# Performance work log

Hardware: AMD Instinct MI355X
Metric: run time of the kernel (lower is better)

Reference implementation:

```python
import jax, jax.numpy as jnp
import numpy as np

T, B, F, H, TAG = 512, 512, 128, 512, 2


def setup_inputs() -> dict:
    key = jax.random.key(0)
    ks = jax.random.split(key, 11)
    s = 1.0 / np.sqrt(H)  # PyTorch LSTMCell/Linear init scale
    u = lambda k, shape: jax.random.uniform(k, shape, jnp.float32, -s, s)
    return {
        "signal": jax.random.normal(ks[0], (T, B, F), jnp.float32),
        "W_ih1": u(ks[1], (4 * H, F)),
        "W_hh1": u(ks[2], (4 * H, H)),
        "b_ih1": u(ks[3], (4 * H,)),
        "b_hh1": u(ks[4], (4 * H,)),
        "W_ih2": u(ks[5], (4 * H, H)),
        "W_hh2": u(ks[6], (4 * H, H)),
        "b_ih2": u(ks[7], (4 * H,)),
        "b_hh2": u(ks[8], (4 * H,)),
        "W_lin": u(ks[9], (TAG, H)),
        "b_lin": u(ks[10], (TAG,)),
    }


def _lstm_cell(x, h, c, W_ih, W_hh, b_ih, b_hh):
    # PyTorch LSTMCell: gates = x W_ih^T + b_ih + h W_hh^T + b_hh; chunks i,f,g,o
    gates = x @ W_ih.T + h @ W_hh.T + (b_ih + b_hh)
    i, f, g, o = jnp.split(gates, 4, axis=-1)
    c_new = jax.nn.sigmoid(f) * c + jax.nn.sigmoid(i) * jnp.tanh(g)
    h_new = jax.nn.sigmoid(o) * jnp.tanh(c_new)
    return h_new, c_new


def reference(signal, W_ih1, W_hh1, b_ih1, b_hh1, W_ih2, W_hh2, b_ih2, b_hh2, W_lin, b_lin):
    n = signal.shape[1]
    hdim = W_hh1.shape[1]
    zeros = jnp.zeros((n, hdim), jnp.float32)

    def step(carry, x_t):
        h1, c1, h2, c2 = carry
        h1, c1 = _lstm_cell(x_t, h1, c1, W_ih1, W_hh1, b_ih1, b_hh1)
        h2, c2 = _lstm_cell(h1, h2, c2, W_ih2, W_hh2, b_ih2, b_hh2)
        out = h2 @ W_lin.T + b_lin  # [B, TAG]
        return (h1, c1, h2, c2), out

    _, outs = jax.lax.scan(step, (zeros, zeros, zeros, zeros), signal)
    # torch.cat(outputs, dim=1): list of T tensors [B, TAG] -> [B, T*TAG]
    t, b, tag = outs.shape
    return jnp.transpose(outs, (1, 0, 2)).reshape(b, t * tag)
```

## Files before the change

kernel.cpp:

```cpp
#include <hip/hip_runtime.h>
#include <hip/hip_fp16.h>
#include <stdint.h>

#define TSTEPS 512
#define BATCH  512
#define FEAT   128
#define HID    512
#define NGATE  2048

typedef _Float16 half8 __attribute__((ext_vector_type(8)));
typedef _Float16 half4v __attribute__((ext_vector_type(4)));
typedef float    floatx4 __attribute__((ext_vector_type(4)));

#define OFF_WIH1 0u
#define SZ_WIH1  ((unsigned)(NGATE*FEAT*2))
#define OFF_WHH1 (OFF_WIH1+SZ_WIH1)
#define SZ_WHH   ((unsigned)(NGATE*HID*2))
#define OFF_WIH2 (OFF_WHH1+SZ_WHH)
#define OFF_WHH2 (OFF_WIH2+SZ_WHH)
#define OFF_B1   (OFF_WHH2+SZ_WHH)
#define OFF_B2   (OFF_B1+(unsigned)(NGATE*4))
#define OFF_H1   (OFF_B2+(unsigned)(NGATE*4))
#define SZ_H     ((unsigned)(2*BATCH*HID*2))
#define OFF_H2   (OFF_H1+SZ_H)
#define OFF_C1   (OFF_H2+SZ_H)
#define SZ_C     ((unsigned)(BATCH*HID*4))
#define OFF_C2   (OFF_C1+SZ_C)
#define WS_END   (OFF_C2+SZ_C)

#define GLOBAL_AS __attribute__((address_space(1)))
#define LDS_AS    __attribute__((address_space(3)))

__device__ __forceinline__ void gload_lds16(const void* g, void* l) {
  __builtin_amdgcn_global_load_lds((const GLOBAL_AS void*)g, (LDS_AS void*)l, 16, 0, 0);
}

__device__ __forceinline__ half8 ldfrag(const _Float16* S, int r, int ko) {
  const int s = ko ^ (r & 3) ^ ((r >> 2) & 3);
  return *(const half8*)(S + r * 32 + s * 8);
}

__global__ void k_conv4(const float* __restrict__ s, _Float16* __restrict__ d, int n4) {
  int i = blockIdx.x * blockDim.x + threadIdx.x;
  if (i < n4) {
    const float4 v = ((const float4*)s)[i];
    half4v h; h[0] = (_Float16)v.x; h[1] = (_Float16)v.y; h[2] = (_Float16)v.z; h[3] = (_Float16)v.w;
    ((half4v*)d)[i] = h;
  }
}

__global__ void k_bias(const float* __restrict__ a, const float* __restrict__ b,
                       float* __restrict__ d, int n) {
  int i = blockIdx.x * blockDim.x + threadIdx.x;
  if (i < n) d[i] = a[i] + b[i];
}

template<bool XF32, int KX, bool DO_OUT>
__global__ __launch_bounds__(256)
void k_cell(const void* __restrict__ xsrc,
            const _Float16* __restrict__ Wx,
            const _Float16* __restrict__ Wh,
            const float* __restrict__ bias,
            const _Float16* __restrict__ hin,
            _Float16* __restrict__ hout,
            float* __restrict__ cst,
            const float* __restrict__ Wlin,
            const float* __restrict__ blin,
            float* __restrict__ out,
            int tstep)
{
  __shared__ __align__(16) _Float16 As[64 * 32];
  __shared__ __align__(16) _Float16 Bs[64 * 32];
  __shared__ float gs[64][65];
  __shared__ float hs[64][17];

  const int tid  = threadIdx.x;
  const int lane = tid & 63;
  const int wave = tid >> 6;
  const int wm = wave >> 1, wn = wave & 1;
  const int bx = blockIdx.x;
  const int hg = blockIdx.y;

  const int r_st  = tid >> 2;
  const int s_st  = tid & 3;
  const int ko_st = s_st ^ (r_st & 3) ^ ((r_st >> 2) & 3);
  const int arow  = bx * 64 + r_st;
  const int brow  = ((r_st >> 4) * HID) + hg * 16 + (r_st & 15);

  _Float16* AsW = As + wave * 512;
  _Float16* BsW = Bs + wave * 512;

  floatx4 acc[2][2];
  #pragma unroll
  for (int a = 0; a < 2; a++)
    #pragma unroll
    for (int b = 0; b < 2; b++) acc[a][b] = (floatx4){0.f, 0.f, 0.f, 0.f};

  const int fr_a = wm * 32 + (lane & 15);
  const int fr_b = wn * 32 + (lane & 15);
  const int fko  = lane >> 4;

  for (int kt = 0; kt < KX; kt += 32) {
    __syncthreads();
    if constexpr (XF32) {
      const float* xf = (const float*)xsrc + (size_t)arow * KX + kt + ko_st * 8;
      float4 v0 = *(const float4*)xf;
      float4 v1 = *(const float4*)(xf + 4);
      half8 h;
      h[0] = (_Float16)v0.x; h[1] = (_Float16)v0.y; h[2] = (_Float16)v0.z; h[3] = (_Float16)v0.w;
      h[4] = (_Float16)v1.x; h[5] = (_Float16)v1.y; h[6] = (_Float16)v1.z; h[7] = (_Float16)v1.w;
      *(half8*)(As + tid * 8) = h;
    } else {
      const _Float16* xh = (const _Float16*)xsrc + (size_t)arow * KX + kt + ko_st * 8;
      gload_lds16(xh, AsW);
    }
    gload_lds16(Wx + (size_t)brow * KX + kt + ko_st * 8, BsW);
    __syncthreads();
    half8 a0 = ldfrag(As, fr_a, fko);
    half8 a1 = ldfrag(As, fr_a + 16, fko);
    half8 b0 = ldfrag(Bs, fr_b, fko);
    half8 b1 = ldfrag(Bs, fr_b + 16, fko);
    acc[0][0] = __builtin_amdgcn_mfma_f32_16x16x32_f16(a0, b0, acc[0][0], 0, 0, 0);
    acc[0][1] = __builtin_amdgcn_mfma_f32_16x16x32_f16(a0, b1, acc[0][1], 0, 0, 0);
    acc[1][0] = __builtin_amdgcn_mfma_f32_16x16x32_f16(a1, b0, acc[1][0], 0, 0, 0);
    acc[1][1] = __builtin_amdgcn_mfma_f32_16x16x32_f16(a1, b1, acc[1][1], 0, 0, 0);
  }

  for (int kt = 0; kt < HID; kt += 32) {
    __syncthreads();
    gload_lds16(hin + (size_t)arow * HID + kt + ko_st * 8, AsW);
    gload_lds16(Wh + (size_t)brow * HID + kt + ko_st * 8, BsW);
    __syncthreads();
    half8 a0 = ldfrag(As, fr_a, fko);
    half8 a1 = ldfrag(As, fr_a + 16, fko);
    half8 b0 = ldfrag(Bs, fr_b, fko);
    half8 b1 = ldfrag(Bs, fr_b + 16, fko);
    acc[0][0] = __builtin_amdgcn_mfma_f32_16x16x32_f16(a0, b0, acc[0][0], 0, 0, 0);
    acc[0][1] = __builtin_amdgcn_mfma_f32_16x16x32_f16(a0, b1, acc[0][1], 0, 0, 0);
    acc[1][0] = __builtin_amdgcn_mfma_f32_16x16x32_f16(a1, b0, acc[1][0], 0, 0, 0);
    acc[1][1] = __builtin_amdgcn_mfma_f32_16x16x32_f16(a1, b1, acc[1][1], 0, 0, 0);
  }

  #pragma unroll
  for (int mi = 0; mi < 2; mi++)
    #pragma unroll
    for (int ni = 0; ni < 2; ni++) {
      const int row = wm * 32 + mi * 16 + (lane >> 4) * 4;
      const int col = wn * 32 + ni * 16 + (lane & 15);
      #pragma unroll
      for (int r = 0; r < 4; r++) gs[row + r][col] = acc[mi][ni][r];
    }
  __syncthreads();

  for (int it = tid; it < 64 * 16; it += 256) {
    const int b = it >> 4, lc = it & 15;
    const int hcol = hg * 16 + lc;
    const float iv = gs[b][lc]      + bias[hcol];
    const float fv = gs[b][16 + lc] + bias[HID + hcol];
    const float gv = gs[b][32 + lc] + bias[2 * HID + hcol];
    const float ov = gs[b][48 + lc] + bias[3 * HID + hcol];
    const float ig = 1.f / (1.f + __expf(-iv));
    const float fg = 1.f / (1.f + __expf(-fv));
    const float og = 1.f / (1.f + __expf(-ov));
    const float tg = 1.f - 2.f / (__expf(2.f * gv) + 1.f);
    const int gidx = (bx * 64 + b) * HID + hcol;
    const float cn = fg * cst[gidx] + ig * tg;
    const float tc = 1.f - 2.f / (__expf(2.f * cn) + 1.f);
    const float hn = og * tc;
    cst[gidx] = cn;
    hout[gidx] = (_Float16)hn;
    if (DO_OUT) hs[b][lc] = hn;
  }

  if (DO_OUT) {
    __syncthreads();
    if (tid < 128) {
      const int b = tid >> 1, tag = tid & 1;
      float sv = 0.f;
      #pragma unroll
      for (int lc = 0; lc < 16; lc++)
        sv += hs[b][lc] * Wlin[tag * HID + hg * 16 + lc];
      if (hg == 0) sv += blin[tag];
      atomicAdd(&out[(size_t)(bx * 64 + b) * (TSTEPS * 2) + tstep * 2 + tag], sv);
    }
  }
}

extern "C" void kernel_launch(void* const* d_in, const int* in_sizes, int n_in,
                              void* d_out, int out_size, void* d_ws, size_t ws_size,
                              hipStream_t stream)
{
  const float* signal = (const float*)d_in[0];
  const float* Wih1 = (const float*)d_in[1];
  const float* Whh1 = (const float*)d_in[2];
  const float* bih1 = (const float*)d_in[3];
  const float* bhh1 = (const float*)d_in[4];
  const float* Wih2 = (const float*)d_in[5];
  const float* Whh2 = (const float*)d_in[6];
  const float* bih2 = (const float*)d_in[7];
  const float* bhh2 = (const float*)d_in[8];
  const float* Wlin = (const float*)d_in[9];
  const float* blin = (const float*)d_in[10];

  char* ws = (char*)d_ws;
  _Float16* wih1h = (_Float16*)(ws + OFF_WIH1);
  _Float16* whh1h = (_Float16*)(ws + OFF_WHH1);
  _Float16* wih2h = (_Float16*)(ws + OFF_WIH2);
  _Float16* whh2h = (_Float16*)(ws + OFF_WHH2);
  float* b1 = (float*)(ws + OFF_B1);
  float* b2 = (float*)(ws + OFF_B2);
  _Float16* h1 = (_Float16*)(ws + OFF_H1);
  _Float16* h2 = (_Float16*)(ws + OFF_H2);
  float* c1 = (float*)(ws + OFF_C1);
  float* c2 = (float*)(ws + OFF_C2);
  float* out = (float*)d_out;

  hipMemsetAsync(ws + OFF_H1, 0, (size_t)(SZ_H * 2 + SZ_C * 2), stream);
  hipMemsetAsync(d_out, 0, (size_t)out_size * 4, stream);

  const int thr = 256;
  k_conv4<<<(NGATE * FEAT / 4 + thr - 1) / thr, thr, 0, stream>>>(Wih1, wih1h, NGATE * FEAT / 4);
  k_conv4<<<(NGATE * HID  / 4 + thr - 1) / thr, thr, 0, stream>>>(Whh1, whh1h, NGATE * HID / 4);
  k_conv4<<<(NGATE * HID  / 4 + thr - 1) / thr, thr, 0, stream>>>(Wih2, wih2h, NGATE * HID / 4);
  k_conv4<<<(NGATE * HID  / 4 + thr - 1) / thr, thr, 0, stream>>>(Whh2, whh2h, NGATE * HID / 4);
  k_bias<<<(NGATE + thr - 1) / thr, thr, 0, stream>>>(bih1, bhh1, b1, NGATE);
  k_bias<<<(NGATE + thr - 1) / thr, thr, 0, stream>>>(bih2, bhh2, b2, NGATE);

  dim3 grid(8, 32), block(256);
  for (int t = 0; t < TSTEPS; t++) {
    const int pin = t & 1, pout = (t + 1) & 1;
    k_cell<true, FEAT, false><<<grid, block, 0, stream>>>(
        (const void*)(signal + (size_t)t * BATCH * FEAT), wih1h, whh1h, b1,
        h1 + (size_t)pin * BATCH * HID, h1 + (size_t)pout * BATCH * HID, c1,
        nullptr, nullptr, nullptr, t);
    k_cell<false, HID, true><<<grid, block, 0, stream>>>(
        (const void*)(h1 + (size_t)pout * BATCH * HID), wih2h, whh2h, b2,
        h2 + (size_t)pin * BATCH * HID, h2 + (size_t)pout * BATCH * HID, c2,
        Wlin, blin, out, t);
  }
}
```

Before: 14.09 ms.

## Replace per-timestep launches with persistent cooperative LSTM kernel with LDS-resident weights

Replaces the 1024 per-step kernel launches with a single cooperative persistent kernel of 256 blocks. Half the blocks run layer 1 and half run layer 2, with flag counters in global memory so layer 2 at step t overlaps layer 1 at step t+1. Each block pre-swizzles and keeps its slice of the fp16 weights resident in LDS, keeps cell state in registers, and uses a register/LDS ring pipeline for the hidden-state operand. This removes launch overhead and repeated weight reloads, at the cost of spin-wait synchronization and requiring all 256 blocks to be co-resident.

```diff
diff --git a/kernel.cpp b/kernel.cpp
--- a/kernel.cpp
+++ b/kernel.cpp
@@ -6,47 +6,32 @@
 #define BATCH  512
 #define FEAT   128
 #define HID    512
-#define NGATE  2048
 
 typedef _Float16 half8 __attribute__((ext_vector_type(8)));
-typedef _Float16 half4v __attribute__((ext_vector_type(4)));
 typedef float    floatx4 __attribute__((ext_vector_type(4)));
 
-#define OFF_WIH1 0u
-#define SZ_WIH1  ((unsigned)(NGATE*FEAT*2))
-#define OFF_WHH1 (OFF_WIH1+SZ_WIH1)
-#define SZ_WHH   ((unsigned)(NGATE*HID*2))
-#define OFF_WIH2 (OFF_WHH1+SZ_WHH)
-#define OFF_WHH2 (OFF_WIH2+SZ_WHH)
-#define OFF_B1   (OFF_WHH2+SZ_WHH)
-#define OFF_B2   (OFF_B1+(unsigned)(NGATE*4))
-#define OFF_H1   (OFF_B2+(unsigned)(NGATE*4))
-#define SZ_H     ((unsigned)(2*BATCH*HID*2))
-#define OFF_H2   (OFF_H1+SZ_H)
-#define OFF_C1   (OFF_H2+SZ_H)
-#define SZ_C     ((unsigned)(BATCH*HID*4))
-#define OFF_C2   (OFF_C1+SZ_C)
-#define WS_END   (OFF_C2+SZ_C)
+#define NCH1 20
+#define NCH2 32
+#define W1RES_B 81920
+#define W2RES_B 131072
+#define RING_B  8192
+#define SMEM_B  (W2RES_B + 3*RING_B)
+
+#define OFF_W1F  0u
+#define OFF_W2F  2621440u
+#define OFF_B1   6815744u
+#define OFF_B2   6823936u
+#define OFF_H1   6832128u
+#define OFF_H2   7880704u
+#define OFF_CNT1 8929280u
+#define OFF_CNT2 8937472u
+#define WS_END   8945664u
 
 #define GLOBAL_AS __attribute__((address_space(1)))
 #define LDS_AS    __attribute__((address_space(3)))
 
 __device__ __forceinline__ void gload_lds16(const void* g, void* l) {
   __builtin_amdgcn_global_load_lds((const GLOBAL_AS void*)g, (LDS_AS void*)l, 16, 0, 0);
-}
-
-__device__ __forceinline__ half8 ldfrag(const _Float16* S, int r, int ko) {
-  const int s = ko ^ (r & 3) ^ ((r >> 2) & 3);
-  return *(const half8*)(S + r * 32 + s * 8);
-}
-
-__global__ void k_conv4(const float* __restrict__ s, _Float16* __restrict__ d, int n4) {
-  int i = blockIdx.x * blockDim.x + threadIdx.x;
-  if (i < n4) {
-    const float4 v = ((const float4*)s)[i];
-    half4v h; h[0] = (_Float16)v.x; h[1] = (_Float16)v.y; h[2] = (_Float16)v.z; h[3] = (_Float16)v.w;
-    ((half4v*)d)[i] = h;
-  }
 }
 
 __global__ void k_bias(const float* __restrict__ a, const float* __restrict__ b,
@@ -55,133 +40,217 @@
   if (i < n) d[i] = a[i] + b[i];
 }
 
-template<bool XF32, int KX, bool DO_OUT>
-__global__ __launch_bounds__(256)
-void k_cell(const void* __restrict__ xsrc,
-            const _Float16* __restrict__ Wx,
-            const _Float16* __restrict__ Wh,
-            const float* __restrict__ bias,
-            const _Float16* __restrict__ hin,
-            _Float16* __restrict__ hout,
-            float* __restrict__ cst,
-            const float* __restrict__ Wlin,
-            const float* __restrict__ blin,
-            float* __restrict__ out,
-            int tstep)
-{
-  __shared__ __align__(16) _Float16 As[64 * 32];
-  __shared__ __align__(16) _Float16 Bs[64 * 32];
-  __shared__ float gs[64][65];
-  __shared__ float hs[64][17];
-
-  const int tid  = threadIdx.x;
-  const int lane = tid & 63;
-  const int wave = tid >> 6;
-  const int wm = wave >> 1, wn = wave & 1;
-  const int bx = blockIdx.x;
-  const int hg = blockIdx.y;
-
-  const int r_st  = tid >> 2;
-  const int s_st  = tid & 3;
-  const int ko_st = s_st ^ (r_st & 3) ^ ((r_st >> 2) & 3);
-  const int arow  = bx * 64 + r_st;
-  const int brow  = ((r_st >> 4) * HID) + hg * 16 + (r_st & 15);
-
-  _Float16* AsW = As + wave * 512;
-  _Float16* BsW = Bs + wave * 512;
-
-  floatx4 acc[2][2];
-  #pragma unroll
-  for (int a = 0; a < 2; a++)
+__global__ void k_wfrag(const float* __restrict__ wih, const float* __restrict__ whh,
+                        _Float16* __restrict__ dst, int KX) {
+  const int kc = blockIdx.x, hg = blockIdx.y, nch = gridDim.x;
+  const int n = threadIdx.x >> 6, lane = threadIdx.x & 63;
+  const int g  = n*512 + hg*16 + (lane & 15);
+  const int k0 = kc*32 + (lane >> 4)*8;
+  const float* src = (k0 < KX) ? (wih + (size_t)g*KX + k0) : (whh + (size_t)g*512 + (k0 - KX));
+  float4 u0 = *(const float4*)src;
+  float4 u1 = *(const float4*)(src + 4);
+  half8 v;
+  v[0]=(_Float16)u0.x; v[1]=(_Float16)u0.y; v[2]=(_Float16)u0.z; v[3]=(_Float16)u0.w;
+  v[4]=(_Float16)u1.x; v[5]=(_Float16)u1.y; v[6]=(_Float16)u1.z; v[7]=(_Float16)u1.w;
+  *(half8*)(dst + ((((size_t)hg*nch + kc)*4 + n)*64 + lane)*8) = v;
+}
+
+__device__ __forceinline__ void sync_wait(int* p, int target) {
+  if (threadIdx.x == 0) {
+    while (__hip_atomic_load(p, __ATOMIC_RELAXED, __HIP_MEMORY_SCOPE_AGENT) < target)
+      __builtin_amdgcn_s_sleep(2);
+  }
+  __syncthreads();
+  __threadfence();
+}
+__device__ __forceinline__ void sync_pub(int* p) {
+  __syncthreads();
+  if (threadIdx.x == 0) { __threadfence(); atomicAdd(p, 1); }
+}
+
+__device__ __forceinline__ void chunk_mfma(const _Float16* ring, int buf, const _Float16* wres,
+                                           int kcb, int rb0, int fko, int lane, floatx4 acc[2][4]) {
+  const _Float16* rb = ring + buf*4096;
+  const int rb1 = rb0 + 16;
+  half8 a0 = *(const half8*)(rb + rb0*32 + (fko ^ (rb0 & 3) ^ ((rb0 >> 2) & 3))*8);
+  half8 a1 = *(const half8*)(rb + rb1*32 + (fko ^ (rb1 & 3) ^ ((rb1 >> 2) & 3))*8);
+  const _Float16* bb = wres + (size_t)kcb*2048 + lane*8;
+  #pragma unroll
+  for (int n = 0; n < 4; ++n) {
+    half8 b = *(const half8*)(bb + n*512);
+    acc[0][n] = __builtin_amdgcn_mfma_f32_16x16x32_f16(a0, b, acc[0][n], 0, 0, 0);
+    acc[1][n] = __builtin_amdgcn_mfma_f32_16x16x32_f16(a1, b, acc[1][n], 0, 0, 0);
+  }
+}
+
+template<int NC>
+__device__ __forceinline__ void kloop_pipe(
+    const _Float16* a0lo, const _Float16* a0hi,
+    const _Float16* a1lo, const _Float16* a1hi,
+    int split, int kcb0,
+    _Float16* ring, int lo0, int lo1,
+    const _Float16* wres, int rb0, int fko, int lane, floatx4 acc[2][4])
+{
+  half8 pa[NC], pb[NC];
+  auto LD = [&](int kc) {
+    const _Float16* pA = (kc < split) ? a0lo : a0hi;
+    const _Float16* pB = (kc < split) ? a1lo : a1hi;
+    pa[kc] = *(const half8*)(pA + kc*32);
+    pb[kc] = *(const half8*)(pB + kc*32);
+  };
+  auto DSW = [&](int kc) {
+    _Float16* d = ring + (kc % 3)*4096;
+    *(half8*)(d + lo0) = pa[kc];
+    *(half8*)(d + lo1) = pb[kc];
+  };
+  LD(0); DSW(0);
+  if (NC > 1) LD(1);
+  #pragma unroll
+  for (int kc = 0; kc < NC; ++kc) {
+    if (kc + 2 < NC) LD(kc + 2);
+    chunk_mfma(ring, kc % 3, wres, kcb0 + kc, rb0, fko, lane, acc);
+    if (kc + 1 < NC) DSW(kc + 1);
+  }
+}
+
+__device__ __forceinline__ void cell_epilogue(const floatx4 acc[2][4], float* creg, float* hnv,
+    float b_i, float b_f, float b_g, float b_o,
+    _Float16* __restrict__ hout, int rowbase, int lane, int hcol)
+{
+  #pragma unroll
+  for (int ci = 0; ci < 8; ++ci) {
+    const int ml = ci >> 2, q = ci & 3;
+    float iv = acc[ml][0][q] + b_i;
+    float fv = acc[ml][1][q] + b_f;
+    float gv = acc[ml][2][q] + b_g;
+    float ov = acc[ml][3][q] + b_o;
+    float ig = 1.f/(1.f+__expf(-iv));
+    float fg = 1.f/(1.f+__expf(-fv));
+    float og = 1.f/(1.f+__expf(-ov));
+    float tg = 1.f - 2.f/(__expf(2.f*gv)+1.f);
+    float cn = fg*creg[ci] + ig*tg;
+    creg[ci] = cn;
+    float tc = 1.f - 2.f/(__expf(2.f*cn)+1.f);
+    float hv = og*tc;
+    hnv[ci] = hv;
+    int rowc = rowbase + ml*16 + (lane >> 4)*4 + q;
+    hout[(size_t)rowc*HID + hcol] = (_Float16)hv;
+  }
+}
+
+__global__ __launch_bounds__(256, 1)
+void lstm_persist(const float* __restrict__ sig,
+                  const _Float16* __restrict__ w1f, const _Float16* __restrict__ w2f,
+                  const float* __restrict__ bias1, const float* __restrict__ bias2,
+                  _Float16* __restrict__ h1b, _Float16* __restrict__ h2b,
+                  int* __restrict__ cnt1, int* __restrict__ cnt2,
+                  const float* __restrict__ Wlin, const float* __restrict__ blin,
+                  float* __restrict__ out)
+{
+  __shared__ __align__(16) char smem[SMEM_B];
+  const int tid = threadIdx.x, lane = tid & 63, w = tid >> 6;
+  const int gid = blockIdx.x;
+  const bool g2 = gid >= 128;
+  const int lg = g2 ? gid - 128 : gid;
+  const int bx = lg >> 5, hg = lg & 31;
+
+  _Float16* wres = (_Float16*)smem;
+  _Float16* ring = (_Float16*)(smem + (g2 ? W2RES_B : W1RES_B));
+
+  {
+    const _Float16* wsrc = g2 ? (w2f + (size_t)hg * (NCH2*4*64*8))
+                              : (w1f + (size_t)hg * (NCH1*4*64*8));
+    const int nj = g2 ? (W2RES_B/4096) : (W1RES_B/4096);
+    for (int j = 0; j < nj; ++j) {
+      char* dst = smem + ((size_t)j*256 + w*64) * 16;
+      gload_lds16(wsrc + ((size_t)j*256 + tid)*8, dst);
+    }
+  }
+  __syncthreads();
+
+  const int hcol = hg*16 + (lane & 15);
+  const float* bias = g2 ? bias2 : bias1;
+  const float b_i = bias[hcol], b_f = bias[512+hcol], b_g = bias[1024+hcol], b_o = bias[1536+hcol];
+  float wl0 = 0.f, wl1 = 0.f, bl0 = 0.f, bl1 = 0.f;
+  if (g2) { wl0 = Wlin[hcol]; wl1 = Wlin[512+hcol]; bl0 = blin[0]; bl1 = blin[1]; }
+
+  const int r0 = 32*w + (lane >> 2), r1 = r0 + 16;
+  const int ss = lane & 3;
+  const int ko0 = ss ^ (r0 & 3) ^ ((r0 >> 2) & 3);
+  const int ko1 = ss ^ (r1 & 3) ^ ((r1 >> 2) & 3);
+  const int lo0 = r0*32 + ss*8, lo1 = r1*32 + ss*8;
+  const int rowg0 = bx*128 + r0, rowg1 = bx*128 + r1;
+  const int hofs0 = rowg0*512 + ko0*8, hofs1 = rowg1*512 + ko1*8;
+
+  const int rb0 = 32*w + (lane & 15);
+  const int fko = lane >> 4;
+  const int rowbase = bx*128 + 32*w;
+
+  float creg[8];
+  #pragma unroll
+  for (int i = 0; i < 8; ++i) creg[i] = 0.f;
+
+  for (int t = 0; t < TSTEPS; ++t) {
+    floatx4 acc[2][4];
     #pragma unroll
-    for (int b = 0; b < 2; b++) acc[a][b] = (floatx4){0.f, 0.f, 0.f, 0.f};
-
-  const int fr_a = wm * 32 + (lane & 15);
-  const int fr_b = wn * 32 + (lane & 15);
-  const int fko  = lane >> 4;
-
-  for (int kt = 0; kt < KX; kt += 32) {
-    __syncthreads();
-    if constexpr (XF32) {
-      const float* xf = (const float*)xsrc + (size_t)arow * KX + kt + ko_st * 8;
-      float4 v0 = *(const float4*)xf;
-      float4 v1 = *(const float4*)(xf + 4);
-      half8 h;
-      h[0] = (_Float16)v0.x; h[1] = (_Float16)v0.y; h[2] = (_Float16)v0.z; h[3] = (_Float16)v0.w;
-      h[4] = (_Float16)v1.x; h[5] = (_Float16)v1.y; h[6] = (_Float16)v1.z; h[7] = (_Float16)v1.w;
-      *(half8*)(As + tid * 8) = h;
+    for (int a = 0; a < 2; ++a)
+      #pragma unroll
+      for (int b = 0; b < 4; ++b) acc[a][b] = (floatx4){0.f, 0.f, 0.f, 0.f};
+
+    const int pin = t & 1, pout = (t + 1) & 1;
+
+    if (!g2) {
+      const float* sigt = sig + (size_t)t * (BATCH*FEAT);
+      #pragma unroll
+      for (int kc = 0; kc < 4; ++kc) {
+        const float* x0 = sigt + rowg0*128 + kc*32 + ko0*8;
+        const float* x1 = sigt + rowg1*128 + kc*32 + ko1*8;
+        float4 u0 = *(const float4*)x0, u1 = *(const float4*)(x0 + 4);
+        float4 u2 = *(const float4*)x1, u3 = *(const float4*)(x1 + 4);
+        half8 v0, v1;
+        v0[0]=(_Float16)u0.x; v0[1]=(_Float16)u0.y; v0[2]=(_Float16)u0.z; v0[3]=(_Float16)u0.w;
+        v0[4]=(_Float16)u1.x; v0[5]=(_Float16)u1.y; v0[6]=(_Float16)u1.z; v0[7]=(_Float16)u1.w;
+        v1[0]=(_Float16)u2.x; v1[1]=(_Float16)u2.y; v1[2]=(_Float16)u2.z; v1[3]=(_Float16)u2.w;
+        v1[4]=(_Float16)u3.x; v1[5]=(_Float16)u3.y; v1[6]=(_Float16)u3.z; v1[7]=(_Float16)u3.w;
+        _Float16* d = ring + (kc % 3)*4096;
+        *(half8*)(d + lo0) = v0;
+        *(half8*)(d + lo1) = v1;
+        chunk_mfma(ring, kc % 3, wres, kc, rb0, fko, lane, acc);
+      }
+      if (t >= 1) sync_wait(&cnt1[(t-1)*4 + bx], 32);
+      if (t >= 2) sync_wait(&cnt2[(t-2)*4 + bx], 32);
+      const _Float16* hprev = h1b + (size_t)pin * (BATCH*HID);
+      kloop_pipe<16>(hprev + hofs0, hprev + hofs0,
+                     hprev + hofs1, hprev + hofs1,
+                     16, 4, ring, lo0, lo1, wres, rb0, fko, lane, acc);
+      _Float16* hout = h1b + (size_t)pout * (BATCH*HID);
+      float hnv[8];
+      cell_epilogue(acc, creg, hnv, b_i, b_f, b_g, b_o, hout, rowbase, lane, hcol);
+      sync_pub(&cnt1[t*4 + bx]);
     } else {
-      const _Float16* xh = (const _Float16*)xsrc + (size_t)arow * KX + kt + ko_st * 8;
-      gload_lds16(xh, AsW);
-    }
-    gload_lds16(Wx + (size_t)brow * KX + kt + ko_st * 8, BsW);
-    __syncthreads();
-    half8 a0 = ldfrag(As, fr_a, fko);
-    half8 a1 = ldfrag(As, fr_a + 16, fko);
-    half8 b0 = ldfrag(Bs, fr_b, fko);
-    half8 b1 = ldfrag(Bs, fr_b + 16, fko);
-    acc[0][0] = __builtin_amdgcn_mfma_f32_16x16x32_f16(a0, b0, acc[0][0], 0, 0, 0);
-    acc[0][1] = __builtin_amdgcn_mfma_f32_16x16x32_f16(a0, b1, acc[0][1], 0, 0, 0);
-    acc[1][0] = __builtin_amdgcn_mfma_f32_16x16x32_f16(a1, b0, acc[1][0], 0, 0, 0);
-    acc[1][1] = __builtin_amdgcn_mfma_f32_16x16x32_f16(a1, b1, acc[1][1], 0, 0, 0);
-  }
-
-  for (int kt = 0; kt < HID; kt += 32) {
-    __syncthreads();
-    gload_lds16(hin + (size_t)arow * HID + kt + ko_st * 8, AsW);
-    gload_lds16(Wh + (size_t)brow * HID + kt + ko_st * 8, BsW);
-    __syncthreads();
-    half8 a0 = ldfrag(As, fr_a, fko);
-    half8 a1 = ldfrag(As, fr_a + 16, fko);
-    half8 b0 = ldfrag(Bs, fr_b, fko);
-    half8 b1 = ldfrag(Bs, fr_b + 16, fko);
-    acc[0][0] = __builtin_amdgcn_mfma_f32_16x16x32_f16(a0, b0, acc[0][0], 0, 0, 0);
-    acc[0][1] = __builtin_amdgcn_mfma_f32_16x16x32_f16(a0, b1, acc[0][1], 0, 0, 0);
-    acc[1][0] = __builtin_amdgcn_mfma_f32_16x16x32_f16(a1, b0, acc[1][0], 0, 0, 0);
-    acc[1][1] = __builtin_amdgcn_mfma_f32_16x16x32_f16(a1, b1, acc[1][1], 0, 0, 0);
-  }
-
-  #pragma unroll
-  for (int mi = 0; mi < 2; mi++)
-    #pragma unroll
-    for (int ni = 0; ni < 2; ni++) {
-      const int row = wm * 32 + mi * 16 + (lane >> 4) * 4;
-      const int col = wn * 32 + ni * 16 + (lane & 15);
+      sync_wait(&cnt1[t*4 + bx], 32);
+      if (t >= 1) sync_wait(&cnt2[(t-1)*4 + bx], 32);
+      const _Float16* h1cur  = h1b + (size_t)pout * (BATCH*HID);
+      const _Float16* h2prev = h2b + (size_t)pin  * (BATCH*HID);
+      kloop_pipe<32>(h1cur + hofs0, h2prev + hofs0 - 16*32,
+                     h1cur + hofs1, h2prev + hofs1 - 16*32,
+                     16, 0, ring, lo0, lo1, wres, rb0, fko, lane, acc);
+      _Float16* hout = h2b + (size_t)pout * (BATCH*HID);
+      float hnv[8];
+      cell_epilogue(acc, creg, hnv, b_i, b_f, b_g, b_o, hout, rowbase, lane, hcol);
+      sync_pub(&cnt2[t*4 + bx]);
       #pragma unroll
-      for (int r = 0; r < 4; r++) gs[row + r][col] = acc[mi][ni][r];
-    }
-  __syncthreads();
-
-  for (int it = tid; it < 64 * 16; it += 256) {
-    const int b = it >> 4, lc = it & 15;
-    const int hcol = hg * 16 + lc;
-    const float iv = gs[b][lc]      + bias[hcol];
-    const float fv = gs[b][16 + lc] + bias[HID + hcol];
-    const float gv = gs[b][32 + lc] + bias[2 * HID + hcol];
-    const float ov = gs[b][48 + lc] + bias[3 * HID + hcol];
-    const float ig = 1.f / (1.f + __expf(-iv));
-    const float fg = 1.f / (1.f + __expf(-fv));
-    const float og = 1.f / (1.f + __expf(-ov));
-    const float tg = 1.f - 2.f / (__expf(2.f * gv) + 1.f);
-    const int gidx = (bx * 64 + b) * HID + hcol;
-    const float cn = fg * cst[gidx] + ig * tg;
-    const float tc = 1.f - 2.f / (__expf(2.f * cn) + 1.f);
-    const float hn = og * tc;
-    cst[gidx] = cn;
-    hout[gidx] = (_Float16)hn;
-    if (DO_OUT) hs[b][lc] = hn;
-  }
-
-  if (DO_OUT) {
-    __syncthreads();
-    if (tid < 128) {
-      const int b = tid >> 1, tag = tid & 1;
-      float sv = 0.f;
-      #pragma unroll
-      for (int lc = 0; lc < 16; lc++)
-        sv += hs[b][lc] * Wlin[tag * HID + hg * 16 + lc];
-      if (hg == 0) sv += blin[tag];
-      atomicAdd(&out[(size_t)(bx * 64 + b) * (TSTEPS * 2) + tstep * 2 + tag], sv);
+      for (int ci = 0; ci < 8; ++ci) {
+        float v0 = hnv[ci]*wl0, v1 = hnv[ci]*wl1;
+        #pragma unroll
+        for (int m = 8; m >= 1; m >>= 1) { v0 += __shfl_xor(v0, m); v1 += __shfl_xor(v1, m); }
+        if ((lane & 15) == 0) {
+          if (hg == 0) { v0 += bl0; v1 += bl1; }
+          const int rowc = rowbase + (ci >> 2)*16 + (lane >> 4)*4 + (ci & 3);
+          atomicAdd(&out[(size_t)rowc*(TSTEPS*2) + t*2 + 0], v0);
+          atomicAdd(&out[(size_t)rowc*(TSTEPS*2) + t*2 + 1], v1);
+        }
+      }
     }
   }
 }
@@ -203,39 +272,26 @@
   const float* blin = (const float*)d_in[10];
 
   char* ws = (char*)d_ws;
-  _Float16* wih1h = (_Float16*)(ws + OFF_WIH1);
-  _Float16* whh1h = (_Float16*)(ws + OFF_WHH1);
-  _Float16* wih2h = (_Float16*)(ws + OFF_WIH2);
-  _Float16* whh2h = (_Float16*)(ws + OFF_WHH2);
+  _Float16* w1f = (_Float16*)(ws + OFF_W1F);
+  _Float16* w2f = (_Float16*)(ws + OFF_W2F);
   float* b1 = (float*)(ws + OFF_B1);
   float* b2 = (float*)(ws + OFF_B2);
   _Float16* h1 = (_Float16*)(ws + OFF_H1);
   _Float16* h2 = (_Float16*)(ws + OFF_H2);
-  float* c1 = (float*)(ws + OFF_C1);
-  float* c2 = (float*)(ws + OFF_C2);
+  int* cnt1 = (int*)(ws + OFF_CNT1);
+  int* cnt2 = (int*)(ws + OFF_CNT2);
   float* out = (float*)d_out;
 
-  hipMemsetAsync(ws + OFF_H1, 0, (size_t)(SZ_H * 2 + SZ_C * 2), stream);
+  hipMemsetAsync(ws + OFF_H1, 0, (size_t)(WS_END - OFF_H1), stream);
   hipMemsetAsync(d_out, 0, (size_t)out_size * 4, stream);
 
-  const int thr = 256;
-  k_conv4<<<(NGATE * FEAT / 4 + thr - 1) / thr, thr, 0, stream>>>(Wih1, wih1h, NGATE * FEAT / 4);
-  k_conv4<<<(NGATE * HID  / 4 + thr - 1) / thr, thr, 0, stream>>>(Whh1, whh1h, NGATE * HID / 4);
-  k_conv4<<<(NGATE * HID  / 4 + thr - 1) / thr, thr, 0, stream>>>(Wih2, wih2h, NGATE * HID / 4);
-  k_conv4<<<(NGATE * HID  / 4 + thr - 1) / thr, thr, 0, stream>>>(Whh2, whh2h, NGATE * HID / 4);
-  k_bias<<<(NGATE + thr - 1) / thr, thr, 0, stream>>>(bih1, bhh1, b1, NGATE);
-  k_bias<<<(NGATE + thr - 1) / thr, thr, 0, stream>>>(bih2, bhh2, b2, NGATE);
-
-  dim3 grid(8, 32), block(256);
-  for (int t = 0; t < TSTEPS; t++) {
-    const int pin = t & 1, pout = (t + 1) & 1;
-    k_cell<true, FEAT, false><<<grid, block, 0, stream>>>(
-        (const void*)(signal + (size_t)t * BATCH * FEAT), wih1h, whh1h, b1,
-        h1 + (size_t)pin * BATCH * HID, h1 + (size_t)pout * BATCH * HID, c1,
-        nullptr, nullptr, nullptr, t);
-    k_cell<false, HID, true><<<grid, block, 0, stream>>>(
-        (const void*)(h1 + (size_t)pout * BATCH * HID), wih2h, whh2h, b2,
-        h2 + (size_t)pin * BATCH * HID, h2 + (size_t)pout * BATCH * HID, c2,
-        Wlin, blin, out, t);
-  }
-}
+  k_wfrag<<<dim3(NCH1, 32), 256, 0, stream>>>(Wih1, Whh1, w1f, FEAT);
+  k_wfrag<<<dim3(NCH2, 32), 256, 0, stream>>>(Wih2, Whh2, w2f, HID);
+  k_bias<<<(2048 + 255) / 256, 256, 0, stream>>>(bih1, bhh1, b1, 2048);
+  k_bias<<<(2048 + 255) / 256, 256, 0, stream>>>(bih2, bhh2, b2, 2048);
+
+  void* args[] = { (void*)&signal, (void*)&w1f, (void*)&w2f, (void*)&b1, (void*)&b2,
+                   (void*)&h1, (void*)&h2, (void*)&cnt1, (void*)&cnt2,
+                   (void*)&Wlin, (void*)&blin, (void*)&out };
+  hipLaunchCooperativeKernel((void*)lstm_persist, dim3(256), dim3(256), args, 0, stream);
+}
```

Result: slower. 28.49 ms (+102.3%).
